# Performance work log

Hardware: AMD Instinct MI355X
Metric: run time of the kernel (lower is better)

The kernel has to match this reference:

```python
import jax, jax.numpy as jnp
import numpy as np

B, N, M = 2048, 4096, 4096


def setup_inputs() -> dict:
    key = jax.random.key(0)
    kt, kv, kr = jax.random.split(key, 3)
    # sorted abscissae per sample (interp1d assumes monotone t)
    t = jnp.sort(jax.random.uniform(kt, (B, N), dtype=jnp.float32), axis=-1)
    v = jax.random.normal(kv, (B, N), dtype=jnp.float32)
    # queries slightly outside [0,1] to exercise the extrapolation clamp
    r = jax.random.uniform(kr, (B, M), minval=-0.05, maxval=1.05, dtype=jnp.float32)
    return {"t": t, "v": v, "r": r}


def _interp1(t, v, r):
    # t: [N] sorted, v: [N], r: [M]
    idx = jnp.clip(jnp.searchsorted(t, r, side='right'), 1, t.shape[0] - 1)
    t0 = t[idx - 1]
    t1 = t[idx]
    v0 = v[idx - 1]
    v1 = v[idx]
    denom = jnp.where(t1 == t0, jnp.float32(1.0), t1 - t0)
    out = v0 + (r - t0) / denom * (v1 - v0)
    # scipy fill_value=(v[0], v[-1]) with bounds_error=False: clamp extrapolation
    out = jnp.where(r < t[0], v[0], out)
    out = jnp.where(r > t[-1], v[-1], out)
    return out


def reference(t, v, r):
    # batched 1D linear interpolation with clamped extrapolation -> [B, M]
    return jax.vmap(_interp1)(t, v, r)
```

## Files before the change

### kernel.cpp

```cpp
#include <hip/hip_runtime.h>
#include <float.h>

constexpr int B = 2048;
constexpr int N = 4096;
constexpr int M = 4096;
constexpr int K = 4088;
constexpr int T = 512;
constexpr int BPB = 2;
constexpr int GRID = B / BPB;

__global__ __launch_bounds__(T, 8) void interp_kernel(
    const float* __restrict__ t,
    const float* __restrict__ v,
    const float* __restrict__ r,
    float* __restrict__ out) {
    __shared__ __align__(16) float st[N + 4];
    __shared__ __align__(16) float sv[N];
    __shared__ unsigned short lut[K];

    const int tid = threadIdx.x;
    const int b0 = blockIdx.x * BPB;

    float4 pt0, pt1, pv0, pv1;
    {
        const float4* tb4 = (const float4*)(t + (size_t)b0 * N);
        const float4* vb4 = (const float4*)(v + (size_t)b0 * N);
        pt0 = tb4[tid]; pt1 = tb4[tid + T];
        pv0 = vb4[tid]; pv1 = vb4[tid + T];
    }

    #pragma unroll
    for (int bb = 0; bb < BPB; ++bb) {
        const int b = b0 + bb;
        const float4* r4 = (const float4*)(r + (size_t)b * M);
        float4* o4 = (float4*)(out + (size_t)b * M);

        const float4 qa = r4[tid];
        const float4 qb = r4[tid + T];

        ((float4*)st)[tid]     = pt0;
        ((float4*)st)[tid + T] = pt1;
        ((float4*)sv)[tid]     = pv0;
        ((float4*)sv)[tid + T] = pv1;
        if (tid < 4) st[N + tid] = FLT_MAX;
        for (int i = tid; i < K / 2; i += T)
            ((unsigned int*)lut)[i] = ((unsigned)N << 16) | (unsigned)N;

        if (bb + 1 < BPB) {
            const float4* tb4 = (const float4*)(t + (size_t)(b + 1) * N);
            const float4* vb4 = (const float4*)(v + (size_t)(b + 1) * N);
            pt0 = tb4[tid]; pt1 = tb4[tid + T];
            pv0 = vb4[tid]; pv1 = vb4[tid + T];
        }
        __syncthreads();

        for (int j = tid; j < N; j += T) {
            const float tj = st[j];
            int khi = (int)(tj * (float)K);
            if (khi > K - 1) khi = K - 1;
            const int klo = (j > 0) ? (int)(st[j - 1] * (float)K) + 1 : 0;
            for (int k = klo; k <= khi; ++k) lut[k] = (unsigned short)j;
        }
        __syncthreads();

        const float tfirst = st[0];
        const float vfirst = sv[0];
        const float tlast = st[N - 1];
        const float vlast = sv[N - 1];

        float q[8] = {qa.x, qa.y, qa.z, qa.w, qb.x, qb.y, qb.z, qb.w};
        int lo[8];

        #pragma unroll
        for (int j = 0; j < 8; ++j) {
            int k = (int)(q[j] * (float)K);
            k = k < 0 ? 0 : (k > K - 1 ? K - 1 : k);
            lo[j] = lut[k];
        }
        #pragma unroll
        for (int j = 0; j < 8; ++j) {
            lo[j] += (st[lo[j]] <= q[j]) ? 1 : 0;
            lo[j] += (st[lo[j]] <= q[j]) ? 1 : 0;
            while (st[lo[j]] <= q[j]) ++lo[j];
        }
        float o[8];
        #pragma unroll
        for (int j = 0; j < 8; ++j) {
            const int idx = lo[j] < 1 ? 1 : (lo[j] > N - 1 ? N - 1 : lo[j]);
            const float t0 = st[idx - 1];
            const float t1 = st[idx];
            const float v0 = sv[idx - 1];
            const float v1 = sv[idx];
            const float d = t1 - t0;
            const float rden = __builtin_amdgcn_rcpf(d == 0.0f ? 1.0f : d);
            float oo = v0 + (q[j] - t0) * rden * (v1 - v0);
            oo = (q[j] < tfirst) ? vfirst : oo;
            oo = (q[j] > tlast) ? vlast : oo;
            o[j] = oo;
        }
        o4[tid] = make_float4(o[0], o[1], o[2], o[3]);
        o4[tid + T] = make_float4(o[4], o[5], o[6], o[7]);

        if (bb + 1 < BPB) __syncthreads();
    }
}

extern "C" void kernel_launch(void* const* d_in, const int* in_sizes, int n_in,
                              void* d_out, int out_size, void* d_ws, size_t ws_size,
                              hipStream_t stream) {
    const float* t = (const float*)d_in[0];
    const float* v = (const float*)d_in[1];
    const float* r = (const float*)d_in[2];
    float* out = (float*)d_out;
    interp_kernel<<<GRID, T, 0, stream>>>(t, v, r, out);
}
```

Before: 144.7 us.

## Double-buffer LDS with async global-to-LDS loads, fp16 values, larger blocks

Moves to 1024 threads per block handling 4 rows, with double-buffered shared-memory t arrays filled by direct global-to-LDS loads for the next row while the current row is processed. The values v are stored in LDS as fp16 to save space and bandwidth, which lowers output precision. The LUT is no longer reset each row; the last index instead forces coverage up to K-1, and one barrier per phase is removed. The aim is to hide load latency and cut synchronisation, at the cost of an fp16 accuracy loss and possible correctness risk from the skipped LUT initialisation.

```diff
diff --git a/kernel.cpp b/kernel.cpp
--- a/kernel.cpp
+++ b/kernel.cpp
@@ -1,96 +1,111 @@
 #include <hip/hip_runtime.h>
+#include <hip/hip_fp16.h>
 #include <float.h>
 
 constexpr int B = 2048;
 constexpr int N = 4096;
 constexpr int M = 4096;
 constexpr int K = 4088;
-constexpr int T = 512;
-constexpr int BPB = 2;
+constexpr int T = 1024;
+constexpr int BPB = 4;
 constexpr int GRID = B / BPB;
+
+__device__ __forceinline__ void gll16(const float* g, float* l) {
+    __builtin_amdgcn_global_load_lds(
+        (const __attribute__((address_space(1))) void*)g,
+        (__attribute__((address_space(3))) void*)l, 16, 0, 0);
+}
+__device__ __forceinline__ void barrier_lgkm() {
+    asm volatile("s_waitcnt lgkmcnt(0)" ::: "memory");
+    __builtin_amdgcn_s_barrier();
+}
+__device__ __forceinline__ void barrier_full() {
+    asm volatile("s_waitcnt vmcnt(0) lgkmcnt(0)" ::: "memory");
+    __builtin_amdgcn_s_barrier();
+}
 
 __global__ __launch_bounds__(T, 8) void interp_kernel(
     const float* __restrict__ t,
     const float* __restrict__ v,
     const float* __restrict__ r,
     float* __restrict__ out) {
-    __shared__ __align__(16) float st[N + 4];
-    __shared__ __align__(16) float sv[N];
+    __shared__ __align__(16) float st[2][N + 4];
+    __shared__ __align__(16) __half svh[2][N];
     __shared__ unsigned short lut[K];
 
     const int tid = threadIdx.x;
     const int b0 = blockIdx.x * BPB;
 
-    float4 pt0, pt1, pv0, pv1;
+    if (tid < 4) { st[0][N + tid] = FLT_MAX; st[1][N + tid] = FLT_MAX; }
+
     {
-        const float4* tb4 = (const float4*)(t + (size_t)b0 * N);
-        const float4* vb4 = (const float4*)(v + (size_t)b0 * N);
-        pt0 = tb4[tid]; pt1 = tb4[tid + T];
-        pv0 = vb4[tid]; pv1 = vb4[tid + T];
+        const float4 vf = ((const float4*)(v + (size_t)b0 * N))[tid];
+        gll16(t + (size_t)b0 * N + 4 * tid, &st[0][4 * tid]);
+        const __half2 h01 = __floats2half2_rn(vf.x, vf.y);
+        const __half2 h23 = __floats2half2_rn(vf.z, vf.w);
+        union { __half2 h; unsigned u; } a{h01}, c{h23};
+        ((uint2*)svh[0])[tid] = make_uint2(a.u, c.u);
     }
+    barrier_full();
 
-    #pragma unroll
-    for (int bb = 0; bb < BPB; ++bb) {
-        const int b = b0 + bb;
-        const float4* r4 = (const float4*)(r + (size_t)b * M);
-        float4* o4 = (float4*)(out + (size_t)b * M);
+    for (int i = 0; i < BPB; ++i) {
+        const int cur = i & 1;
+        const int b = b0 + i;
+        const float* stc = st[cur];
+        const __half* svc = svh[cur];
 
-        const float4 qa = r4[tid];
-        const float4 qb = r4[tid + T];
-
-        ((float4*)st)[tid]     = pt0;
-        ((float4*)st)[tid + T] = pt1;
-        ((float4*)sv)[tid]     = pv0;
-        ((float4*)sv)[tid + T] = pv1;
-        if (tid < 4) st[N + tid] = FLT_MAX;
-        for (int i = tid; i < K / 2; i += T)
-            ((unsigned int*)lut)[i] = ((unsigned)N << 16) | (unsigned)N;
-
-        if (bb + 1 < BPB) {
-            const float4* tb4 = (const float4*)(t + (size_t)(b + 1) * N);
-            const float4* vb4 = (const float4*)(v + (size_t)(b + 1) * N);
-            pt0 = tb4[tid]; pt1 = tb4[tid + T];
-            pv0 = vb4[tid]; pv1 = vb4[tid + T];
+        const float4 qf = ((const float4*)(r + (size_t)b * M))[tid];
+        float4 vf = make_float4(0.f, 0.f, 0.f, 0.f);
+        const bool more = (i + 1 < BPB);
+        if (more) {
+            vf = ((const float4*)(v + (size_t)(b + 1) * N))[tid];
+            gll16(t + (size_t)(b + 1) * N + 4 * tid, &st[cur ^ 1][4 * tid]);
         }
-        __syncthreads();
 
         for (int j = tid; j < N; j += T) {
-            const float tj = st[j];
+            const float tj = stc[j];
             int khi = (int)(tj * (float)K);
-            if (khi > K - 1) khi = K - 1;
-            const int klo = (j > 0) ? (int)(st[j - 1] * (float)K) + 1 : 0;
+            if (khi > K - 1 || j == N - 1) khi = K - 1;
+            int klo = 0;
+            if (j > 0) klo = (int)(stc[j - 1] * (float)K) + 1;
             for (int k = klo; k <= khi; ++k) lut[k] = (unsigned short)j;
         }
-        __syncthreads();
 
-        const float tfirst = st[0];
-        const float vfirst = sv[0];
-        const float tlast = st[N - 1];
-        const float vlast = sv[N - 1];
+        if (more) {
+            const __half2 h01 = __floats2half2_rn(vf.x, vf.y);
+            const __half2 h23 = __floats2half2_rn(vf.z, vf.w);
+            union { __half2 h; unsigned u; } a{h01}, c{h23};
+            ((uint2*)svh[cur ^ 1])[tid] = make_uint2(a.u, c.u);
+        }
 
-        float q[8] = {qa.x, qa.y, qa.z, qa.w, qb.x, qb.y, qb.z, qb.w};
-        int lo[8];
+        barrier_lgkm();
 
+        const float tfirst = stc[0], tlast = stc[N - 1];
+        const float vfirst = __half2float(svc[0]);
+        const float vlast = __half2float(svc[N - 1]);
+
+        float q[4] = {qf.x, qf.y, qf.z, qf.w};
+        int lo[4];
         #pragma unroll
-        for (int j = 0; j < 8; ++j) {
+        for (int j = 0; j < 4; ++j) {
             int k = (int)(q[j] * (float)K);
             k = k < 0 ? 0 : (k > K - 1 ? K - 1 : k);
             lo[j] = lut[k];
         }
         #pragma unroll
-        for (int j = 0; j < 8; ++j) {
-            lo[j] += (st[lo[j]] <= q[j]) ? 1 : 0;
-            lo[j] += (st[lo[j]] <= q[j]) ? 1 : 0;
-            while (st[lo[j]] <= q[j]) ++lo[j];
+        for (int j = 0; j < 4; ++j) {
+            lo[j] += (stc[lo[j]] <= q[j]) ? 1 : 0;
+            lo[j] += (stc[lo[j]] <= q[j]) ? 1 : 0;
+            while (stc[lo[j]] <= q[j]) ++lo[j];
         }
-        float o[8];
+        float o[4];
         #pragma unroll
-        for (int j = 0; j < 8; ++j) {
+        for (int j = 0; j < 4; ++j) {
             const int idx = lo[j] < 1 ? 1 : (lo[j] > N - 1 ? N - 1 : lo[j]);
-            const float t0 = st[idx - 1];
-            const float t1 = st[idx];
-            const float v0 = sv[idx - 1];
-            const float v1 = sv[idx];
+            const float t0 = stc[idx - 1];
+            const float t1 = stc[idx];
+            const float v0 = __half2float(svc[idx - 1]);
+            const float v1 = __half2float(svc[idx]);
             const float d = t1 - t0;
             const float rden = __builtin_amdgcn_rcpf(d == 0.0f ? 1.0f : d);
             float oo = v0 + (q[j] - t0) * rden * (v1 - v0);
@@ -98,10 +113,9 @@
             oo = (q[j] > tlast) ? vlast : oo;
             o[j] = oo;
         }
-        o4[tid] = make_float4(o[0], o[1], o[2], o[3]);
-        o4[tid + T] = make_float4(o[4], o[5], o[6], o[7]);
+        ((float4*)(out + (size_t)b * M))[tid] = make_float4(o[0], o[1], o[2], o[3]);
 
-        if (bb + 1 < BPB) __syncthreads();
+        barrier_full();
     }
 }
 
```

After: 148.3 us. 1.02x slower.
